# Kernel tuning notes

Hardware: AMD Instinct MI355X
Metric: run time of the kernel (lower is better)

## Reference

```python
import jax, jax.numpy as jnp
import numpy as np

DIM = 1024

def setup_inputs() -> dict:
    key = jax.random.key(0)
    k1, k2, k3, k4 = jax.random.split(key, 4)
    scale = 1.0 / np.sqrt(DIM)
    return {
        "segment_embeds": jax.random.normal(k1, (32, 2048, DIM), dtype=jnp.float32),
        "Wq": jax.random.normal(k2, (DIM, DIM), dtype=jnp.float32) * scale,
        "bq": jax.random.normal(k3, (DIM,), dtype=jnp.float32) * scale,
        "mem_bank": jax.random.normal(k4, (131072, DIM), dtype=jnp.float32) * scale,
        "k": 8,
    }

def reference(segment_embeds, Wq, bq, mem_bank, k):
    # mean-pool over time: (B, C)
    segment_mean = segment_embeds.mean(axis=1)
    # linear query projection (torch Linear: x @ W.T + b)
    q = segment_mean @ Wq.T + bq
    # dense scores against memory bank: (B, M)
    attn_scores = (q @ mem_bank.T) / jnp.sqrt(jnp.asarray(DIM, dtype=q.dtype))
    # top-k select
    top_k_scores, top_k_indices = jax.lax.top_k(attn_scores, k)  # (B, K)
    attn_weights = jax.nn.softmax(top_k_scores, axis=-1)  # (B, K)
    # gather retrieved vectors: (B, K, C)
    retrieved_vectors = mem_bank[top_k_indices]
    # weighted sum over K, keepdim -> (B, 1, C)
    retrieved_mem = jnp.sum(attn_weights[..., None] * retrieved_vectors, axis=1, keepdims=True)
    return retrieved_mem
```

## Files before the change

### kernel.cpp

```cpp
#include <hip/hip_runtime.h>
#include <hip/hip_bf16.h>
#include <math.h>

#define NB 32
#define NT 2048
#define NC 1024
#define NM 131072
#define TOPK 8
#define MBLK 64
#define SBLOCKS (NM / MBLK)

typedef __attribute__((ext_vector_type(8))) short s16x8;
typedef __attribute__((ext_vector_type(4))) float f32x4;
typedef __attribute__((ext_vector_type(4))) int i32x4;

#define OFF_PART 0
#define OFF_CS   0
#define OFF_CI   524288
#define OFF_MEAN 1048576
#define OFF_Q    (OFF_MEAN + 32768)
#define OFF_QB   (OFF_Q + 32768)

__device__ __forceinline__ unsigned short f2bf(float f) {
    unsigned u = __float_as_uint(f);
    unsigned r = (u + 0x7FFFu + ((u >> 16) & 1u)) >> 16;
    return (unsigned short)r;
}

__global__ __launch_bounds__(256) void mean_partial_k(const float* __restrict__ seg,
                                                      float* __restrict__ part) {
    int blk = blockIdx.x;
    int b = blk >> 5, tc = blk & 31;
    int tid = threadIdx.x;
    const float4* src = (const float4*)(seg + ((size_t)b * NT + (size_t)tc * 64) * NC);
    float4 acc = make_float4(0.f, 0.f, 0.f, 0.f);
#pragma unroll 4
    for (int t = 0; t < 64; ++t) {
        float4 v = src[(size_t)t * 256 + tid];
        acc.x += v.x; acc.y += v.y; acc.z += v.z; acc.w += v.w;
    }
    ((float4*)(part + ((size_t)b * 32 + tc) * NC))[tid] = acc;
}

__global__ __launch_bounds__(256) void mean_finalize_k(const float* __restrict__ part,
                                                       float* __restrict__ mean) {
    int i = blockIdx.x * 256 + threadIdx.x;
    int b = i >> 10, c = i & 1023;
    float s = 0.f;
#pragma unroll
    for (int tc = 0; tc < 32; ++tc) s += part[((size_t)b * 32 + tc) * NC + c];
    mean[i] = s * (1.0f / NT);
}

__global__ __launch_bounds__(256) void qproj_k(const float* __restrict__ mean,
                                               const float* __restrict__ Wq,
                                               const float* __restrict__ bq,
                                               float* __restrict__ q) {
    int wave = (blockIdx.x * 256 + threadIdx.x) >> 6;
    int lane = threadIdx.x & 63;
    int o0 = wave * 16;
    for (int j = 0; j < 16; ++j) {
        int o = o0 + j;
        int b = o >> 10, i = o & 1023;
        const float4* wr = (const float4*)(Wq + (size_t)i * NC);
        const float4* mr = (const float4*)(mean + (size_t)b * NC);
        float acc = 0.f;
#pragma unroll
        for (int e = 0; e < 4; ++e) {
            float4 w4 = wr[lane * 4 + e];
            float4 m4 = mr[lane * 4 + e];
            acc += w4.x * m4.x + w4.y * m4.y + w4.z * m4.z + w4.w * m4.w;
        }
#pragma unroll
        for (int off = 32; off; off >>= 1) acc += __shfl_xor(acc, off);
        if (lane == 0) q[o] = acc + bq[i];
    }
}

__global__ __launch_bounds__(256) void qbf_k(const float* __restrict__ q,
                                             s16x8* __restrict__ qb) {
    int idx = blockIdx.x * 256 + threadIdx.x;
    int lane = idx & 63, n = (idx >> 6) & 1, ks = idx >> 7;
    int b = n * 16 + (lane & 15);
    int k0 = ks * 32 + ((lane >> 4) << 3);
    s16x8 v;
#pragma unroll
    for (int e = 0; e < 8; ++e) v[e] = (short)f2bf(q[(size_t)b * NC + k0 + e]);
    qb[idx] = v;
}

#define BUBBLE8(v, vi, s, si)                                   \
    {                                                           \
        float _v = (v); int _vi = (vi);                         \
        _Pragma("unroll")                                       \
        for (int _u = 0; _u < 8; ++_u) {                        \
            bool _gt = _v > s[_u];                              \
            float _ts = _gt ? _v : s[_u];                       \
            int _ti = _gt ? _vi : si[_u];                       \
            _v = _gt ? s[_u] : _v;                              \
            _vi = _gt ? si[_u] : _vi;                           \
            s[_u] = _ts; si[_u] = _ti;                          \
        }                                                       \
    }

#define BUBBLE8F(v, s)                                          \
    {                                                           \
        float _v = (v);                                         \
        _Pragma("unroll")                                       \
        for (int _u = 0; _u < 8; ++_u) {                        \
            bool _gt = _v > s[_u];                              \
            float _ts = _gt ? _v : s[_u];                       \
            _v = _gt ? s[_u] : _v;                              \
            s[_u] = _ts;                                        \
        }                                                       \
    }

__global__ __launch_bounds__(256, 8) void scores_mfma_k(const float* __restrict__ memb,
                                                        const s16x8* __restrict__ qb,
                                                        float* __restrict__ candS,
                                                        int* __restrict__ candI) {
    __shared__ __align__(16) float smemf[2880];
    int tid = threadIdx.x, lane = tid & 63, wid = tid >> 6;
    int m0 = blockIdx.x * MBLK;

    f32x4 acc[2];
    acc[0] = (f32x4){0.f, 0.f, 0.f, 0.f};
    acc[1] = (f32x4){0.f, 0.f, 0.f, 0.f};

    const unsigned* abase = (const unsigned*)(memb
        + (size_t)(m0 + wid * 16 + (lane & 15)) * NC + ((lane >> 4) << 3));
    uint4 lo0 = *(const uint4*)(abase);
    uint4 hi0 = *(const uint4*)(abase + 4);
    s16x8 bf0 = qb[lane];
    s16x8 bf1 = qb[64 + lane];

    for (int ks = 0; ks < 32; ++ks) {
        uint4 lo1, hi1; s16x8 nb0, nb1;
        if (ks < 31) {
            lo1 = *(const uint4*)(abase + (ks + 1) * 32);
            hi1 = *(const uint4*)(abase + (ks + 1) * 32 + 4);
            nb0 = qb[((ks + 1) * 2 + 0) * 64 + lane];
            nb1 = qb[((ks + 1) * 2 + 1) * 64 + lane];
        }
        __builtin_amdgcn_sched_barrier(0);
        i32x4 ai;
        ai[0] = __builtin_amdgcn_perm(lo0.y, lo0.x, 0x07060302u);
        ai[1] = __builtin_amdgcn_perm(lo0.w, lo0.z, 0x07060302u);
        ai[2] = __builtin_amdgcn_perm(hi0.y, hi0.x, 0x07060302u);
        ai[3] = __builtin_amdgcn_perm(hi0.w, hi0.z, 0x07060302u);
        s16x8 a = __builtin_bit_cast(s16x8, ai);
        acc[0] = __builtin_amdgcn_mfma_f32_16x16x32_bf16(a, bf0, acc[0], 0, 0, 0);
        acc[1] = __builtin_amdgcn_mfma_f32_16x16x32_bf16(a, bf1, acc[1], 0, 0, 0);
        lo0 = lo1; hi0 = hi1; bf0 = nb0; bf1 = nb1;
    }

#pragma unroll
    for (int n = 0; n < 2; ++n)
#pragma unroll
        for (int j = 0; j < 4; ++j) {
            int bb = n * 16 + (lane & 15);
            int mm = wid * 16 + ((lane >> 4) << 2) + j;
            smemf[bb * 65 + mm] = acc[n][j] * 0.03125f;
        }
    __syncthreads();

    {
        int b = tid >> 3, p = tid & 7;
        float s[8];
#pragma unroll
        for (int u = 0; u < 8; ++u) s[u] = -INFINITY;
#pragma unroll
        for (int j = 0; j < 8; ++j) {
            int ml = (p + j * 8 + b * 4) & 63;
            float v = smemf[b * 65 + ml];
            unsigned uu = (__float_as_uint(v) & ~0xFFu) | (unsigned)ml;
            BUBBLE8F(__uint_as_float(uu), s);
        }
        __syncthreads();
        float* cs = smemf;
#pragma unroll
        for (int u = 0; u < 8; ++u) cs[tid * 9 + u] = s[u];
        __syncthreads();
        float* csA = smemf + 2304;
        if (tid < 64) {
            float s2[8];
#pragma unroll
            for (int u = 0; u < 8; ++u) s2[u] = -INFINITY;
            int t0 = (tid >> 1) * 8 + (tid & 1) * 4;
            for (int tt = 0; tt < 4; ++tt)
#pragma unroll
                for (int u = 0; u < 8; ++u)
                    BUBBLE8F(cs[(t0 + tt) * 9 + u], s2);
#pragma unroll
            for (int u = 0; u < 8; ++u) csA[tid * 9 + u] = s2[u];
        }
        __syncthreads();
        if (tid < 32) {
            float s3[8];
#pragma unroll
            for (int u = 0; u < 8; ++u) s3[u] = -INFINITY;
            for (int j = 0; j < 16; ++j)
                BUBBLE8F(csA[(tid * 2 + (j >> 3)) * 9 + (j & 7)], s3);
#pragma unroll
            for (int u = 0; u < 8; ++u) {
                candS[((size_t)tid * SBLOCKS + blockIdx.x) * 8 + u] = s3[u];
                candI[((size_t)tid * SBLOCKS + blockIdx.x) * 8 + u] =
                    m0 + (int)(__float_as_uint(s3[u]) & 0xFFu);
            }
        }
    }
}

__global__ __launch_bounds__(256) void finalize_k(const float* __restrict__ candS,
                                                  const int* __restrict__ candI,
                                                  const float* __restrict__ memb,
                                                  const float* __restrict__ q,
                                                  float* __restrict__ out) {
    __shared__ float cs[256 * 9];
    __shared__ int ci[256 * 9];
    __shared__ float csA[64 * 9];
    __shared__ int ciA[64 * 9];
    __shared__ float exsc[64];
    __shared__ int exid[64];
    __shared__ float wgt[8];
    __shared__ int widx[8];
    int b = blockIdx.x, tid = threadIdx.x;
    const float* S = candS + (size_t)b * (SBLOCKS * 8);
    const int* I = candI + (size_t)b * (SBLOCKS * 8);

    {
        float s[8]; int si[8];
#pragma unroll
        for (int u = 0; u < 8; ++u) { s[u] = -INFINITY; si[u] = -1; }
        for (int j = 0; j < 64; ++j)
            BUBBLE8(S[tid * 64 + j], I[tid * 64 + j], s, si);
#pragma unroll
        for (int u = 0; u < 8; ++u) { cs[tid * 9 + u] = s[u]; ci[tid * 9 + u] = si[u]; }
    }
    __syncthreads();
    if (tid < 64) {
        float s[8]; int si[8];
#pragma unroll
        for (int u = 0; u < 8; ++u) { s[u] = -INFINITY; si[u] = -1; }
        for (int tt = 0; tt < 4; ++tt)
#pragma unroll
            for (int u = 0; u < 8; ++u)
                BUBBLE8(cs[(tid * 4 + tt) * 9 + u], ci[(tid * 4 + tt) * 9 + u], s, si);
#pragma unroll
        for (int u = 0; u < 8; ++u) { csA[tid * 9 + u] = s[u]; ciA[tid * 9 + u] = si[u]; }
    }
    __syncthreads();
    if (tid < 8) {
        float s[8]; int si[8];
#pragma unroll
        for (int u = 0; u < 8; ++u) { s[u] = -INFINITY; si[u] = -1; }
        for (int tt = 0; tt < 8; ++tt)
#pragma unroll
            for (int u = 0; u < 8; ++u)
                BUBBLE8(csA[(tid * 8 + tt) * 9 + u], ciA[(tid * 8 + tt) * 9 + u], s, si);
#pragma unroll
        for (int u = 0; u < 8; ++u) exid[tid * 8 + u] = si[u];
    }
    __syncthreads();
    {
        int w = tid >> 6, lane = tid & 63;
        const float4* qr = (const float4*)(q + (size_t)b * NC);
        for (int i = 0; i < 16; ++i) {
            int c = w * 16 + i;
            int row = exid[c];
            const float4* mr = (const float4*)(memb + (size_t)row * NC);
            float d = 0.f;
#pragma unroll
            for (int e = 0; e < 4; ++e) {
                float4 m4 = mr[e * 64 + lane];
                float4 q4 = qr[e * 64 + lane];
                d += m4.x * q4.x + m4.y * q4.y + m4.z * q4.z + m4.w * q4.w;
            }
#pragma unroll
            for (int off = 32; off; off >>= 1) d += __shfl_xor(d, off);
            if (lane == 0) exsc[c] = d * 0.03125f;
        }
    }
    __syncthreads();
    if (tid == 0) {
        float s4[8]; int si4[8];
#pragma unroll
        for (int u = 0; u < 8; ++u) { s4[u] = -INFINITY; si4[u] = -1; }
        for (int j = 0; j < 64; ++j)
            BUBBLE8(exsc[j], exid[j], s4, si4);
        float m = s4[0], sum = 0.f, w[8];
#pragma unroll
        for (int u = 0; u < 8; ++u) { w[u] = __expf(s4[u] - m); sum += w[u]; }
        float inv = 1.0f / sum;
#pragma unroll
        for (int u = 0; u < 8; ++u) { wgt[u] = w[u] * inv; widx[u] = si4[u]; }
    }
    __syncthreads();
    {
        float wv[8]; int ix[8];
#pragma unroll
        for (int u = 0; u < 8; ++u) { wv[u] = wgt[u]; ix[u] = widx[u]; }
        float4 o = make_float4(0.f, 0.f, 0.f, 0.f);
#pragma unroll
        for (int u = 0; u < 8; ++u) {
            float4 r = ((const float4*)(memb + (size_t)ix[u] * NC))[tid];
            o.x = fmaf(wv[u], r.x, o.x);
            o.y = fmaf(wv[u], r.y, o.y);
            o.z = fmaf(wv[u], r.z, o.z);
            o.w = fmaf(wv[u], r.w, o.w);
        }
        ((float4*)(out + (size_t)b * NC))[tid] = o;
    }
}

extern "C" void kernel_launch(void* const* d_in, const int* in_sizes, int n_in,
                              void* d_out, int out_size, void* d_ws, size_t ws_size,
                              hipStream_t stream) {
    const float* seg  = (const float*)d_in[0];
    const float* Wq   = (const float*)d_in[1];
    const float* bq   = (const float*)d_in[2];
    const float* memb = (const float*)d_in[3];
    float* ws = (float*)d_ws;
    float* part  = ws + OFF_PART;
    float* mean  = ws + OFF_MEAN;
    float* q     = ws + OFF_Q;
    s16x8* qb    = (s16x8*)(ws + OFF_QB);
    float* candS = ws + OFF_CS;
    int*   candI = (int*)(ws + OFF_CI);
    float* out = (float*)d_out;

    mean_partial_k<<<NB * 32, 256, 0, stream>>>(seg, part);
    mean_finalize_k<<<(NB * NC) / 256, 256, 0, stream>>>(part, mean);
    qproj_k<<<512, 256, 0, stream>>>(mean, Wq, bq, q);
    qbf_k<<<16, 256, 0, stream>>>(q, qb);
    scores_mfma_k<<<SBLOCKS, 256, 0, stream>>>(memb, qb, candS, candI);
    finalize_k<<<NB, 256, 0, stream>>>(candS, candI, memb, q, out);
}
```

Measured before the change: 233.2 us.

## Restructure score kernel into persistent blocks with LDS double-buffered async loads

The score kernel goes from 2048 small blocks of 64 rows to 256 blocks, each streaming 512 memory-bank rows in 16-row tiles. Tiles are double-buffered into LDS with global_load_lds, and the K dimension is split across wave pairs. Each block keeps a running top-8 per batch row across tiles, which makes the candidate array eight times smaller and shortens the finalize merge. The cost is three barriers per tile and a single block per CU. The grid of 256 blocks may leave some CUs idle, and occupancy drops, so latency hiding depends on the manual pipeline.

```diff
diff --git a/kernel.cpp b/kernel.cpp
--- a/kernel.cpp
+++ b/kernel.cpp
@@ -7,8 +7,13 @@
 #define NC 1024
 #define NM 131072
 #define TOPK 8
-#define MBLK 64
-#define SBLOCKS (NM / MBLK)
+#define NSB 256
+#define ROWS_PB 512
+#define NP 32
+#define SLOTF 260
+#define TILEF (4 * 16 * SLOTF)
+#define SCOFF (2 * TILEF)
+#define SMEMF (SCOFF + 2 * 32 * 17)
 
 typedef __attribute__((ext_vector_type(8))) short s16x8;
 typedef __attribute__((ext_vector_type(4))) float f32x4;
@@ -16,7 +21,7 @@
 
 #define OFF_PART 0
 #define OFF_CS   0
-#define OFF_CI   524288
+#define OFF_CI   65536
 #define OFF_MEAN 1048576
 #define OFF_Q    (OFF_MEAN + 32768)
 #define OFF_QB   (OFF_Q + 32768)
@@ -25,6 +30,11 @@
     unsigned u = __float_as_uint(f);
     unsigned r = (u + 0x7FFFu + ((u >> 16) & 1u)) >> 16;
     return (unsigned short)r;
+}
+
+__device__ __forceinline__ void gl_lds16(const float* g, float* l) {
+    __builtin_amdgcn_global_load_lds((const __attribute__((address_space(1))) void*)g,
+                                     (__attribute__((address_space(3))) void*)l, 16, 0, 0);
 }
 
 __global__ __launch_bounds__(256) void mean_partial_k(const float* __restrict__ seg,
@@ -94,7 +104,7 @@
         float _v = (v); int _vi = (vi);                         \
         _Pragma("unroll")                                       \
         for (int _u = 0; _u < 8; ++_u) {                        \
-            bool _gt = _v > s[_u];                              \
+            bool _gt = _v > s[_u];                               \
             float _ts = _gt ? _v : s[_u];                       \
             int _ti = _gt ? _vi : si[_u];                       \
             _v = _gt ? s[_u] : _v;                              \
@@ -108,78 +118,100 @@
         float _v = (v);                                         \
         _Pragma("unroll")                                       \
         for (int _u = 0; _u < 8; ++_u) {                        \
-            bool _gt = _v > s[_u];                              \
+            bool _gt = _v > s[_u];                               \
             float _ts = _gt ? _v : s[_u];                       \
             _v = _gt ? s[_u] : _v;                              \
             s[_u] = _ts;                                        \
         }                                                       \
     }
 
-__global__ __launch_bounds__(256, 8) void scores_mfma_k(const float* __restrict__ memb,
+__global__ __launch_bounds__(256, 1) void scores_mfma_k(const float* __restrict__ memb,
                                                         const s16x8* __restrict__ qb,
                                                         float* __restrict__ candS,
                                                         int* __restrict__ candI) {
-    __shared__ __align__(16) float smemf[2880];
-    int tid = threadIdx.x, lane = tid & 63, wid = tid >> 6;
-    int m0 = blockIdx.x * MBLK;
-
-    f32x4 acc[2];
-    acc[0] = (f32x4){0.f, 0.f, 0.f, 0.f};
-    acc[1] = (f32x4){0.f, 0.f, 0.f, 0.f};
-
-    const unsigned* abase = (const unsigned*)(memb
-        + (size_t)(m0 + wid * 16 + (lane & 15)) * NC + ((lane >> 4) << 3));
-    uint4 lo0 = *(const uint4*)(abase);
-    uint4 hi0 = *(const uint4*)(abase + 4);
-    s16x8 bf0 = qb[lane];
-    s16x8 bf1 = qb[64 + lane];
-
-    for (int ks = 0; ks < 32; ++ks) {
-        uint4 lo1, hi1; s16x8 nb0, nb1;
-        if (ks < 31) {
-            lo1 = *(const uint4*)(abase + (ks + 1) * 32);
-            hi1 = *(const uint4*)(abase + (ks + 1) * 32 + 4);
-            nb0 = qb[((ks + 1) * 2 + 0) * 64 + lane];
-            nb1 = qb[((ks + 1) * 2 + 1) * 64 + lane];
-        }
-        __builtin_amdgcn_sched_barrier(0);
-        i32x4 ai;
-        ai[0] = __builtin_amdgcn_perm(lo0.y, lo0.x, 0x07060302u);
-        ai[1] = __builtin_amdgcn_perm(lo0.w, lo0.z, 0x07060302u);
-        ai[2] = __builtin_amdgcn_perm(hi0.y, hi0.x, 0x07060302u);
-        ai[3] = __builtin_amdgcn_perm(hi0.w, hi0.z, 0x07060302u);
-        s16x8 a = __builtin_bit_cast(s16x8, ai);
-        acc[0] = __builtin_amdgcn_mfma_f32_16x16x32_bf16(a, bf0, acc[0], 0, 0, 0);
-        acc[1] = __builtin_amdgcn_mfma_f32_16x16x32_bf16(a, bf1, acc[1], 0, 0, 0);
-        lo0 = lo1; hi0 = hi1; bf0 = nb0; bf1 = nb1;
-    }
-
-#pragma unroll
-    for (int n = 0; n < 2; ++n)
-#pragma unroll
-        for (int j = 0; j < 4; ++j) {
-            int bb = n * 16 + (lane & 15);
-            int mm = wid * 16 + ((lane >> 4) << 2) + j;
-            smemf[bb * 65 + mm] = acc[n][j] * 0.03125f;
-        }
-    __syncthreads();
+    extern __shared__ __align__(16) float smemf[];
+    int tid = threadIdx.x, lane = tid & 63, ws = tid >> 6;
+    int n = ws & 1, kh = ws >> 1;
+    size_t mb0 = (size_t)blockIdx.x * ROWS_PB;
+
+    float s8[8];
+#pragma unroll
+    for (int u = 0; u < 8; ++u) s8[u] = -INFINITY;
+
+#define TISSUE(p_) { float* lb = smemf + ((p_) & 1) * TILEF;                          \
+    const float* gb = memb + (mb0 + (size_t)(p_) * 16) * NC + lane * 4;               \
+    _Pragma("unroll") for (int i_ = 0; i_ < 16; ++i_) {                               \
+        int r_ = ws * 4 + (i_ >> 2), c_ = i_ & 3;                                     \
+        gl_lds16(gb + (size_t)r_ * NC + c_ * 256, lb + (c_ * 16 + r_) * SLOTF); } }
+
+    s16x8 qf[16];
+#pragma unroll
+    for (int s = 0; s < 16; ++s)
+        qf[s] = qb[((kh * 16 + s) * 2 + n) * 64 + lane];
+
+    TISSUE(0);
+    TISSUE(1);
+
+    for (int p = 0; p < NP; ++p) {
+        if (p + 1 < NP) { asm volatile("s_waitcnt vmcnt(16)" ::: "memory"); }
+        else            { asm volatile("s_waitcnt vmcnt(0)" ::: "memory"); }
+        __builtin_amdgcn_sched_barrier(0);
+        __builtin_amdgcn_s_barrier();
+        __builtin_amdgcn_sched_barrier(0);
+
+        f32x4 acc = (f32x4){0.f, 0.f, 0.f, 0.f};
+        const float* tb = smemf + (p & 1) * TILEF;
+#pragma unroll
+        for (int s = 0; s < 16; ++s) {
+            int ksg = kh * 16 + s;
+            const float* ap = tb + ((ksg >> 3) * 16 + (lane & 15)) * SLOTF
+                            + (ksg & 7) * 32 + ((lane >> 4) << 3);
+            uint4 lo = *(const uint4*)(ap);
+            uint4 hi = *(const uint4*)(ap + 4);
+            i32x4 ai;
+            ai[0] = __builtin_amdgcn_perm(lo.y, lo.x, 0x07060302u);
+            ai[1] = __builtin_amdgcn_perm(lo.w, lo.z, 0x07060302u);
+            ai[2] = __builtin_amdgcn_perm(hi.y, hi.x, 0x07060302u);
+            ai[3] = __builtin_amdgcn_perm(hi.w, hi.z, 0x07060302u);
+            s16x8 a = __builtin_bit_cast(s16x8, ai);
+            acc = __builtin_amdgcn_mfma_f32_16x16x32_bf16(a, qf[s], acc, 0, 0, 0);
+        }
+
+        {
+            int bcol = n * 16 + (lane & 15);
+            int mrow = (lane >> 4) << 2;
+#pragma unroll
+            for (int j = 0; j < 4; ++j)
+                smemf[SCOFF + (kh * 32 + bcol) * 17 + mrow + j] = acc[j];
+        }
+        asm volatile("s_waitcnt lgkmcnt(0)" ::: "memory");
+        __builtin_amdgcn_sched_barrier(0);
+        __builtin_amdgcn_s_barrier();
+        __builtin_amdgcn_sched_barrier(0);
+
+        {
+            int b = tid >> 3, pq = tid & 7;
+#pragma unroll
+            for (int rr = 0; rr < 2; ++rr) {
+                int m = pq + rr * 8;
+                float v = smemf[SCOFF + b * 17 + m]
+                        + smemf[SCOFF + (32 + b) * 17 + m];
+                unsigned uu = (__float_as_uint(v) & ~0x1FFu) | (unsigned)(p * 16 + m);
+                BUBBLE8F(__uint_as_float(uu), s8);
+            }
+        }
+        __builtin_amdgcn_sched_barrier(0);
+        __builtin_amdgcn_s_barrier();
+        __builtin_amdgcn_sched_barrier(0);
+
+        if (p + 2 < NP) TISSUE(p + 2);
+    }
+#undef TISSUE
 
     {
-        int b = tid >> 3, p = tid & 7;
-        float s[8];
-#pragma unroll
-        for (int u = 0; u < 8; ++u) s[u] = -INFINITY;
-#pragma unroll
-        for (int j = 0; j < 8; ++j) {
-            int ml = (p + j * 8 + b * 4) & 63;
-            float v = smemf[b * 65 + ml];
-            unsigned uu = (__float_as_uint(v) & ~0xFFu) | (unsigned)ml;
-            BUBBLE8F(__uint_as_float(uu), s);
-        }
-        __syncthreads();
         float* cs = smemf;
 #pragma unroll
-        for (int u = 0; u < 8; ++u) cs[tid * 9 + u] = s[u];
+        for (int u = 0; u < 8; ++u) cs[tid * 9 + u] = s8[u];
         __syncthreads();
         float* csA = smemf + 2304;
         if (tid < 64) {
@@ -203,9 +235,9 @@
                 BUBBLE8F(csA[(tid * 2 + (j >> 3)) * 9 + (j & 7)], s3);
 #pragma unroll
             for (int u = 0; u < 8; ++u) {
-                candS[((size_t)tid * SBLOCKS + blockIdx.x) * 8 + u] = s3[u];
-                candI[((size_t)tid * SBLOCKS + blockIdx.x) * 8 + u] =
-                    m0 + (int)(__float_as_uint(s3[u]) & 0xFFu);
+                candS[((size_t)tid * NSB + blockIdx.x) * 8 + u] = s3[u] * 0.03125f;
+                candI[((size_t)tid * NSB + blockIdx.x) * 8 + u] =
+                    (int)mb0 + (int)(__float_as_uint(s3[u]) & 0x1FFu);
             }
         }
     }
@@ -225,15 +257,15 @@
     __shared__ float wgt[8];
     __shared__ int widx[8];
     int b = blockIdx.x, tid = threadIdx.x;
-    const float* S = candS + (size_t)b * (SBLOCKS * 8);
-    const int* I = candI + (size_t)b * (SBLOCKS * 8);
+    const float* S = candS + (size_t)b * (NSB * 8);
+    const int* I = candI + (size_t)b * (NSB * 8);
 
     {
         float s[8]; int si[8];
 #pragma unroll
         for (int u = 0; u < 8; ++u) { s[u] = -INFINITY; si[u] = -1; }
-        for (int j = 0; j < 64; ++j)
-            BUBBLE8(S[tid * 64 + j], I[tid * 64 + j], s, si);
+        for (int j = 0; j < 8; ++j)
+            BUBBLE8(S[tid * 8 + j], I[tid * 8 + j], s, si);
 #pragma unroll
         for (int u = 0; u < 8; ++u) { cs[tid * 9 + u] = s[u]; ci[tid * 9 + u] = si[u]; }
     }
@@ -329,10 +361,14 @@
     int*   candI = (int*)(ws + OFF_CI);
     float* out = (float*)d_out;
 
+    (void)hipFuncSetAttribute((const void*)scores_mfma_k,
+                              hipFuncAttributeMaxDynamicSharedMemorySize,
+                              SMEMF * 4);
+
     mean_partial_k<<<NB * 32, 256, 0, stream>>>(seg, part);
     mean_finalize_k<<<(NB * NC) / 256, 256, 0, stream>>>(part, mean);
     qproj_k<<<512, 256, 0, stream>>>(mean, Wq, bq, q);
     qbf_k<<<16, 256, 0, stream>>>(q, qb);
-    scores_mfma_k<<<SBLOCKS, 256, 0, stream>>>(memb, qb, candS, candI);
+    scores_mfma_k<<<NSB, 256, SMEMF * 4, stream>>>(memb, qb, candS, candI);
     finalize_k<<<NB, 256, 0, stream>>>(candS, candI, memb, q, out);
 }
```

Measured after the change: 204.6 us (median of 3 runs). 1.14x faster.
